# Kernel optimization log

Measured on AMD Instinct MI355X. Metric: run time of the kernel, lower is better.

The kernel has to match this reference:

```python
import jax, jax.numpy as jnp
import numpy as np
import math

N = 20000          # real nodes (batch_size)
D = 256            # hidden_dim
H = 4              # num_heads
L = 3              # num_layers
E = 320000         # local edges
EXP_DEG = 4        # expander_degree
LN_EPS = 1e-5


def setup_inputs() -> dict:
    key = jax.random.key(0)
    ks = jax.random.split(key, 8)
    x = jax.random.normal(ks[0], (N, D), jnp.float32)
    rng = np.random.default_rng(0)
    edge_index = jnp.asarray(rng.integers(0, N, size=(2, E)), dtype=jnp.int32)
    # Expander: EXP_DEG//2 random permutations on N+1 nodes (incl. virtual node),
    # each contributing edges in both directions -> degree-EXP_DEG regular graph.
    n = N + 1
    perms = [rng.permutation(n) for _ in range(EXP_DEG // 2)]
    src = np.concatenate([np.arange(n) for _ in perms] + perms)
    dst = np.concatenate(perms + [np.arange(n) for _ in perms])
    exp_edge_index = jnp.asarray(np.stack([src, dst]), dtype=jnp.int32)
    s_in = 1.0 / math.sqrt(D)
    s_ffn = 1.0 / math.sqrt(4 * D)
    def w(k, shape, s):
        return jax.random.normal(k, shape, jnp.float32) * s
    params = {
        'Wqkv_loc': w(ks[1], (L, D, 3 * D), s_in), 'bqkv_loc': jnp.zeros((L, 3 * D), jnp.float32),
        'Wo_loc':   w(ks[2], (L, D, D), s_in),     'bo_loc':   jnp.zeros((L, D), jnp.float32),
        'Wqkv_exp': w(ks[3], (L, D, 3 * D), s_in), 'bqkv_exp': jnp.zeros((L, 3 * D), jnp.float32),
        'Wo_exp':   w(ks[4], (L, D, D), s_in),     'bo_exp':   jnp.zeros((L, D), jnp.float32),
        'ln_g': jnp.ones((L, D), jnp.float32),     'ln_b': jnp.zeros((L, D), jnp.float32),
        'W1': w(ks[5], (L, D, 4 * D), s_in),       'b1': jnp.zeros((L, 4 * D), jnp.float32),
        'W2': w(ks[6], (L, 4 * D, D), s_ffn),      'b2': jnp.zeros((L, D), jnp.float32),
    }
    return {'x': x, 'edge_index': edge_index, 'exp_edge_index': exp_edge_index, **params}


def _attention(h, src, dst, Wqkv, bqkv, Wo, bo):
    # Sparse multi-head attention over (src -> dst) edges with segment softmax per dst.
    n, d = h.shape
    dh = d // H
    qkv = (h @ Wqkv + bqkv).reshape(n, 3, H, dh)
    q, k, v = qkv[:, 0], qkv[:, 1], qkv[:, 2]            # [n, H, dh]
    score = (q[dst] * k[src]).sum(-1) / jnp.sqrt(jnp.float32(dh))  # [e, H]
    m = jax.ops.segment_max(score, dst, num_segments=n)  # [n, H]
    ex = jnp.exp(score - m[dst])
    denom = jax.ops.segment_sum(ex, dst, num_segments=n)
    alpha = ex / (denom[dst] + 1e-16)
    out = jax.ops.segment_sum(alpha[:, :, None] * v[src], dst, num_segments=n)  # [n, H, dh]
    return out.reshape(n, d) @ Wo + bo


def _layer_norm(x, g, b):
    mu = x.mean(-1, keepdims=True)
    var = ((x - mu) ** 2).mean(-1, keepdims=True)
    return (x - mu) * jax.lax.rsqrt(var + LN_EPS) * g + b


def reference(x, edge_index, exp_edge_index, Wqkv_loc, bqkv_loc, Wo_loc, bo_loc,
              Wqkv_exp, bqkv_exp, Wo_exp, bo_exp, ln_g, ln_b, W1, b1, W2, b2):
    n0 = x.shape[0]
    # VirtualNode transform: append one zero-feature node connected to/from all nodes.
    h = jnp.concatenate([x, jnp.zeros((1, x.shape[1]), x.dtype)], axis=0)
    ar = jnp.arange(n0, dtype=edge_index.dtype)
    vn = jnp.full((n0,), n0, dtype=edge_index.dtype)
    src = jnp.concatenate([edge_index[0], ar, vn])
    dst = jnp.concatenate([edge_index[1], vn, ar])
    esrc, edst = exp_edge_index[0], exp_edge_index[1]
    for l in range(L):  # fixed small number of structurally distinct layers
        res = h
        loc = _attention(h, src, dst, Wqkv_loc[l], bqkv_loc[l], Wo_loc[l], bo_loc[l])
        exp = _attention(h, esrc, edst, Wqkv_exp[l], bqkv_exp[l], Wo_exp[l], bo_exp[l])
        h = _layer_norm(res + loc + exp, ln_g[l], ln_b[l])
        h = h + (jax.nn.gelu(h @ W1[l] + b1[l], approximate=False) @ W2[l] + b2[l])
    return h[:n0]
```

## Files before the change

### kernel.cpp

```cpp
#include <hip/hip_runtime.h>
#include <stdint.h>

#define NREAL   20000
#define NNODES  20001
#define VN      20000
#define E_EDGES 320000
#define NEXP    80004
#define MPAD    20096
#define NVNW    320

typedef unsigned short u16;
typedef unsigned int   u32;
typedef __bf16 bf16x8 __attribute__((ext_vector_type(8)));
typedef float  f32x4  __attribute__((ext_vector_type(4)));
typedef u16    u16x8  __attribute__((ext_vector_type(8)));

__device__ __host__ __forceinline__ size_t fmoff(int row, int col, int LD) {
    return (size_t)(row >> 4) * ((size_t)LD * 16) + (size_t)((col >> 3) * 128)
         + (size_t)((row & 15) * 8) + (size_t)(col & 7);
}

__device__ __forceinline__ int qkv_perm(int n) {
    if (n < 256) return n;
    int u = n - 256;
    int part = u >> 8;
    int cl = u & 255;
    return 256 + (cl >> 2) * 8 + part * 4 + (cl & 3);
}

__device__ __forceinline__ float bf2f(u16 v) {
    union { u32 u; float f; } x; x.u = ((u32)v) << 16; return x.f;
}
__device__ __forceinline__ u16 f2bf(float f) {
    union { float f; u32 u; } x; x.f = f;
    u32 r = (x.u + 0x7fffu + ((x.u >> 16) & 1u)) >> 16;
    return (u16)r;
}
__device__ __forceinline__ float4 cvt4(ushort4 u) {
    return make_float4(bf2f(u.x), bf2f(u.y), bf2f(u.z), bf2f(u.w));
}
__device__ __forceinline__ float4 ld4bf(const u16* p) { return cvt4(*(const ushort4*)p); }
__device__ __forceinline__ float4 cvtk8(u16x8 r) {
    return make_float4(bf2f(r[0]), bf2f(r[1]), bf2f(r[2]), bf2f(r[3]));
}
__device__ __forceinline__ float4 cvtv8(u16x8 r) {
    return make_float4(bf2f(r[4]), bf2f(r[5]), bf2f(r[6]), bf2f(r[7]));
}


__global__ void hinit_kernel(const float* __restrict__ x, float* __restrict__ h,
                             u16* __restrict__ hb) {
    int idx = blockIdx.x * 256 + threadIdx.x;
    if (idx >= NNODES * 64) return;
    int row = idx >> 6, c0 = (idx & 63) * 4;
    float4 v = make_float4(0.f, 0.f, 0.f, 0.f);
    if (row < NREAL) v = *(const float4*)(x + (size_t)row * 256 + c0);
    *(float4*)(h + (size_t)row * 256 + c0) = v;
    ushort4 o;
    o.x = f2bf(v.x); o.y = f2bf(v.y); o.z = f2bf(v.z); o.w = f2bf(v.w);
    *(ushort4*)(hb + fmoff(row, c0, 256)) = o;
}

__global__ void init_kernel(int* cnt, int* fill, int* ecnt,
                            const float* __restrict__ bl, const float* __restrict__ be,
                            float* __restrict__ bcat,
                            const float* __restrict__ bol, const float* __restrict__ boe,
                            float* __restrict__ bsum) {
    int i = blockIdx.x * 256 + threadIdx.x;
    if (i < NREAL) { cnt[i] = 0; fill[i] = 0; }
    if (i < NNODES) ecnt[i] = 0;
    if (i < 3 * 1536) {
        int l = i / 1536, c = i - l * 1536;
        float v = (c < 768) ? bl[l * 768 + c] : be[l * 768 + c - 768];
        int cc = (c >= 768) ? c - 768 : c;
        int d = qkv_perm(cc) + ((c >= 768) ? 768 : 0);
        bcat[l * 1536 + d] = v;
    }
    if (i < 3 * 256) bsum[i] = bol[i] + boe[i];
}

__global__ void csr_count_kernel(const int* __restrict__ ei, int* __restrict__ cnt) {
    int e = blockIdx.x * 256 + threadIdx.x;
    if (e < E_EDGES) atomicAdd(&cnt[ei[E_EDGES + e]], 1);
}

__global__ void csr_scan_kernel(const int* __restrict__ cnt, int* __restrict__ indptr) {
    __shared__ int ssum[256];
    int t = threadIdx.x;
    int c0 = t * 79;
    int s = 0;
    for (int j = 0; j < 79; j++) {
        int i = c0 + j;
        if (i < NREAL) s += cnt[i];
    }
    ssum[t] = s;
    __syncthreads();
    for (int d2 = 1; d2 < 256; d2 <<= 1) {
        int v = (t >= d2) ? ssum[t - d2] : 0;
        __syncthreads();
        ssum[t] += v;
        __syncthreads();
    }
    int run = (t == 0) ? 0 : ssum[t - 1];
    for (int j = 0; j < 79; j++) {
        int i = c0 + j;
        if (i < NREAL) { indptr[i] = run; run += cnt[i]; }
    }
    if (t == 255) indptr[NREAL] = run;
}

__global__ void csr_scatter_kernel(const int* __restrict__ ei, const int* __restrict__ indptr,
                                   int* __restrict__ fill, int* __restrict__ srcs) {
    int e = blockIdx.x * 256 + threadIdx.x;
    if (e < E_EDGES) {
        int d = ei[E_EDGES + e];
        int pos = indptr[d] + atomicAdd(&fill[d], 1);
        srcs[pos] = ei[e];
    }
}

__global__ void exp_scatter_kernel(const int* __restrict__ eei, int* __restrict__ ecnt,
                                   int* __restrict__ esrcs) {
    int e = blockIdx.x * 256 + threadIdx.x;
    if (e < NEXP) {
        int d = eei[NEXP + e];
        int pos = atomicAdd(&ecnt[d], 1);
        esrcs[d * 4 + pos] = eei[e];
    }
}

__global__ void wconv_all_kernel(const float* __restrict__ WqkvL, const float* __restrict__ WqkvE,
                                 const float* __restrict__ WoL, const float* __restrict__ WoE,
                                 const float* __restrict__ W1, const float* __restrict__ W2,
                                 u16* __restrict__ out) {
    int i = blockIdx.x * 256 + threadIdx.x;
    if (i >= 3 * 1048576) return;
    int l = i / 1048576, r = i - l * 1048576;
    if (r >= 393216 && r < 524288) {
        int r2 = r - 393216;
        int k = r2 >> 8, n = r2 & 255;
        float v = (k < 256) ? WoL[(size_t)l * 65536 + k * 256 + n]
                            : WoE[(size_t)l * 65536 + (k - 256) * 256 + n];
        out[(size_t)l * 1048576 + 393216 + fmoff(n, k, 512)] = f2bf(v);
        return;
    }
    const float* src; int K, N; int base;
    if (r < 196608)      { src = WqkvL; K = 256;  N = 768;  base = 0; }
    else if (r < 393216) { src = WqkvE; K = 256;  N = 768;  base = 196608; }
    else if (r < 786432) { src = W1;    K = 256;  N = 1024; base = 524288; }
    else                 { src = W2;    K = 1024; N = 256;  base = 786432; }
    int r2 = r - base;
    int k = r2 / N, n = r2 - k * N;
    int d = (r < 393216) ? qkv_perm(n) : n;
    out[(size_t)l * 1048576 + base + fmoff(d, k, K)] = f2bf(src[(size_t)l * K * N + r2]);
}

template <int EPI>
__global__ __launch_bounds__(256) void gemm_bn(
    const u16* __restrict__ A, const u16* __restrict__ Bt, const float* __restrict__ bias,
    u16* Cb, u16* Q0, u16* KV0, u16* Q1, u16* KV1, int M, int Nout, int nbn) {
    __shared__ u16 lB[128 * 256];
    const int lin = blockIdx.x;
    const int xcd = lin & 7, rest = lin >> 3;
    const int nt = rest % nbn, mc = xcd + 8 * (rest / nbn);
    const int tn = nt * 128;
    const int tid = threadIdx.x;
    const int w = tid >> 6, lane = tid & 63;
    const int lm = lane & 15, q = lane >> 4;

    {
        const u16* bsrc = Bt + (size_t)(tn >> 4) * 4096;
#pragma unroll
        for (int r = 0; r < 16; r++) {
            int o = (r * 256 + tid) * 8;
            *(bf16x8*)&lB[o] = *(const bf16x8*)&bsrc[o];
        }
    }
    __syncthreads();

    f32x4 acc[2][8];
#pragma unroll
    for (int a = 0; a < 2; a++)
#pragma unroll
        for (int b = 0; b < 8; b++) acc[a][b] = (f32x4)0.0f;

    const int lbo = q * 128 + lm * 8;
    const int maxp = MPAD / 16 - 1;

    bf16x8 aS[3][2], bS[2][8];
#pragma unroll
    for (int s = 0; s < 2; s++) {
        int p0 = (mc * 4) * 8 + w * 2;
#pragma unroll
        for (int f = 0; f < 2; f++) {
            int p = p0 + f; if (p > maxp) p = maxp;
            aS[s][f] = *(const bf16x8*)(A + (size_t)p * 4096 + s * 512 + lbo);
        }
#pragma unroll
        for (int n = 0; n < 8; n++)
            bS[s][n] = *(const bf16x8*)&lB[n * 4096 + s * 512 + lbo];
    }

#pragma unroll
    for (int t = 0; t < 32; t++) {
        const int mt = t >> 3, kk = t & 7;
        if (t + 2 < 32) {
            const int t2 = t + 2, mt2 = t2 >> 3, kk2 = t2 & 7;
            int p0 = (mc * 4 + mt2) * 8 + w * 2;
#pragma unroll
            for (int f = 0; f < 2; f++) {
                int p = p0 + f; if (p > maxp) p = maxp;
                aS[t2 % 3][f] = *(const bf16x8*)(A + (size_t)p * 4096 + kk2 * 512 + lbo);
            }
        }
        if (t >= 1 && t + 1 < 32) {
            const int kk1 = (t + 1) & 7;
#pragma unroll
            for (int n = 0; n < 8; n++)
                bS[(t + 1) & 1][n] = *(const bf16x8*)&lB[n * 4096 + kk1 * 512 + lbo];
        }
#pragma unroll
        for (int mi = 0; mi < 2; mi++)
#pragma unroll
            for (int ni = 0; ni < 8; ni++)
                acc[mi][ni] = __builtin_amdgcn_mfma_f32_16x16x32_bf16(
                    bS[t & 1][ni], aS[t % 3][mi], acc[mi][ni], 0, 0, 0);

        if (kk == 7) {
            const int tmg = (mc * 4 + mt) * 128;
#pragma unroll
            for (int mi = 0; mi < 2; mi++) {
                int grow = tmg + w * 32 + mi * 16 + lm;
                if (grow < M) {
#pragma unroll
                    for (int ni = 0; ni < 8; ni++) {
                        int gcol = tn + ni * 16 + q * 4;
                        float4 b4 = *(const float4*)(bias + gcol);
                        float v0 = acc[mi][ni][0] + b4.x;
                        float v1 = acc[mi][ni][1] + b4.y;
                        float v2 = acc[mi][ni][2] + b4.z;
                        float v3 = acc[mi][ni][3] + b4.w;
                        ushort4 o;
                        o.x = f2bf(v0); o.y = f2bf(v1); o.z = f2bf(v2); o.w = f2bf(v3);
                        u16* dst;
                        if (gcol < 256)       dst = Q0  + (size_t)grow * 256 + gcol;
                        else if (gcol < 768)  dst = KV0 + (size_t)grow * 512 + (gcol - 256);
                        else if (gcol < 1024) dst = Q1  + (size_t)grow * 256 + (gcol - 768);
                        else                  dst = KV1 + (size_t)grow * 512 + (gcol - 1024);
                        *(ushort4*)dst = o;
                    }
                }
#pragma unroll
                for (int ni = 0; ni < 8; ni++) acc[mi][ni] = (f32x4)0.0f;
            }
        }
    }
}

__global__ __launch_bounds__(256) void ffn1_rw(
    const u16* __restrict__ A, const u16* __restrict__ Bt, const float* __restrict__ bias,
    u16* __restrict__ Cb, int M) {
    const int lin = blockIdx.x;
    const int mt = lin >> 2, ns = lin & 3;
    const int tm = mt * 64;
    if (tm >= M) return;
    const int tid = threadIdx.x;
    const int w = tid >> 6, lane = tid & 63;
    const int lm = lane & 15, q = lane >> 4;

    f32x4 acc[4][4];
#pragma unroll
    for (int a = 0; a < 4; a++)
#pragma unroll
        for (int b = 0; b < 4; b++) acc[a][b] = (f32x4)0.0f;

    const u16* apf[4];
    const u16* bpf[4];
#pragma unroll
    for (int mi = 0; mi < 4; mi++)
        apf[mi] = A + (size_t)(tm / 16 + mi) * 4096 + q * 128 + lm * 8;
#pragma unroll
    for (int ni = 0; ni < 4; ni++)
        bpf[ni] = Bt + (size_t)(ns * 16 + w * 4 + ni) * 4096 + q * 128 + lm * 8;

    bf16x8 sA[3][4], sB[3][4];
#pragma unroll
    for (int s = 0; s < 2; s++) {
#pragma unroll
        for (int mi = 0; mi < 4; mi++) sA[s][mi] = *(const bf16x8*)(apf[mi] + s * 512);
#pragma unroll
        for (int ni = 0; ni < 4; ni++) sB[s][ni] = *(const bf16x8*)(bpf[ni] + s * 512);
    }
#pragma unroll
    for (int i = 0; i < 8; i++) {
        const int cu = i % 3, pf = (i + 2) % 3;
        if (i + 2 < 8) {
#pragma unroll
            for (int mi = 0; mi < 4; mi++) sA[pf][mi] = *(const bf16x8*)(apf[mi] + (i + 2) * 512);
#pragma unroll
            for (int ni = 0; ni < 4; ni++) sB[pf][ni] = *(const bf16x8*)(bpf[ni] + (i + 2) * 512);
        }
#pragma unroll
        for (int mi = 0; mi < 4; mi++)
#pragma unroll
            for (int ni = 0; ni < 4; ni++)
                acc[mi][ni] = __builtin_amdgcn_mfma_f32_16x16x32_bf16(
                    sB[cu][ni], sA[cu][mi], acc[mi][ni], 0, 0, 0);
    }

    float4 b4[4];
#pragma unroll
    for (int ni = 0; ni < 4; ni++)
        b4[ni] = *(const float4*)(bias + ns * 256 + w * 64 + ni * 16 + q * 4);

#pragma unroll
    for (int mi = 0; mi < 4; mi++) {
        int grow = tm + mi * 16 + lm;
        if (grow >= M) continue;
#pragma unroll
        for (int ni = 0; ni < 4; ni++) {
            int gcol = ns * 256 + w * 64 + ni * 16 + q * 4;
            float v0 = acc[mi][ni][0] + b4[ni].x;
            float v1 = acc[mi][ni][1] + b4[ni].y;
            float v2 = acc[mi][ni][2] + b4[ni].z;
            float v3 = acc[mi][ni][3] + b4[ni].w;
            float g0, g1, g2, g3;
            {
                float u = 0.7978845608f * (v0 + 0.044715f * v0 * v0 * v0);
                g0 = 0.5f * v0 * (2.0f - 2.0f / (__expf(2.0f * u) + 1.0f));
            }
            {
                float u = 0.7978845608f * (v1 + 0.044715f * v1 * v1 * v1);
                g1 = 0.5f * v1 * (2.0f - 2.0f / (__expf(2.0f * u) + 1.0f));
            }
            {
                float u = 0.7978845608f * (v2 + 0.044715f * v2 * v2 * v2);
                g2 = 0.5f * v2 * (2.0f - 2.0f / (__expf(2.0f * u) + 1.0f));
            }
            {
                float u = 0.7978845608f * (v3 + 0.044715f * v3 * v3 * v3);
                g3 = 0.5f * v3 * (2.0f - 2.0f / (__expf(2.0f * u) + 1.0f));
            }
            ushort4 o;
            o.x = f2bf(g0); o.y = f2bf(g1); o.z = f2bf(g2); o.w = f2bf(g3);
            *(ushort4*)(Cb + fmoff(grow, gcol, 1024)) = o;
        }
    }
}

template <int EPI, int K, int MT>
__global__ __launch_bounds__(256) void gemm_fm(
    const u16* __restrict__ A, const u16* __restrict__ Bt, const float* __restrict__ bias,
    u16* Cb, float* Cf, const float* resid, int M, int Nout, int nby) {
    constexpr int MFR = MT / 32;
    constexpr int NK = K / 32;
    const int lin = blockIdx.x;
    const int xcd = lin & 7, sub = lin >> 3;
    const int mtile = xcd + 8 * (sub / nby);
    const int ntile = sub - (sub / nby) * nby;
    const int tm = mtile * MT, tn = ntile * 128;
    if (tm >= M) return;

    const int tid = threadIdx.x;
    const int w = tid >> 6, lane = tid & 63;
    const int lm = lane & 15, q = lane >> 4;
    const int mo = (w >> 1) * (MT / 2), no = (w & 1) * 64;

    f32x4 acc[MFR][4];
#pragma unroll
    for (int a = 0; a < MFR; a++)
#pragma unroll
        for (int b = 0; b < 4; b++) acc[a][b] = (f32x4)0.0f;

    const u16* apf[MFR];
    const u16* bpf[4];
#pragma unroll
    for (int t = 0; t < MFR; t++) {
        int p = (tm + mo) / 16 + t;
        apf[t] = A + (size_t)p * (16 * K) + q * 128 + lm * 8;
    }
#pragma unroll
    for (int n = 0; n < 4; n++) {
        int c = (tn + no) / 16 + n;
        bpf[n] = Bt + (size_t)c * (16 * K) + q * 128 + lm * 8;
    }

    bf16x8 sA[3][MFR], sB[3][4];
#pragma unroll
    for (int s = 0; s < 2 && s < NK; s++) {
#pragma unroll
        for (int t = 0; t < MFR; t++) sA[s][t] = *(const bf16x8*)(apf[t] + s * 512);
#pragma unroll
        for (int n = 0; n < 4; n++) sB[s][n] = *(const bf16x8*)(bpf[n] + s * 512);
    }
#pragma unroll
    for (int i = 0; i < NK; i++) {
        const int cu = i % 3, pf = (i + 2) % 3;
        if (i + 2 < NK) {
#pragma unroll
            for (int t = 0; t < MFR; t++) sA[pf][t] = *(const bf16x8*)(apf[t] + (i + 2) * 512);
#pragma unroll
            for (int n = 0; n < 4; n++) sB[pf][n] = *(const bf16x8*)(bpf[n] + (i + 2) * 512);
        }
#pragma unroll
        for (int mi = 0; mi < MFR; mi++)
#pragma unroll
            for (int ni = 0; ni < 4; ni++)
                acc[mi][ni] = __builtin_amdgcn_mfma_f32_16x16x32_bf16(
                    sB[cu][ni], sA[cu][mi], acc[mi][ni], 0, 0, 0);
    }

    float4 b4[4];
#pragma unroll
    for (int ni = 0; ni < 4; ni++)
        b4[ni] = *(const float4*)(bias + tn + no + ni * 16 + q * 4);

#pragma unroll
    for (int mi = 0; mi < MFR; mi++) {
        int grow = tm + mo + mi * 16 + lm;
        if constexpr (EPI == 4) { if (grow >= NREAL) continue; }
        else                    { if (grow >= M) continue; }
#pragma unroll
        for (int ni = 0; ni < 4; ni++) {
            int gcol = tn + no + ni * 16 + q * 4;
            float v0 = acc[mi][ni][0] + b4[ni].x;
            float v1 = acc[mi][ni][1] + b4[ni].y;
            float v2 = acc[mi][ni][2] + b4[ni].z;
            float v3 = acc[mi][ni][3] + b4[ni].w;
            size_t idx = (size_t)grow * Nout + gcol;
            if constexpr (EPI == 1) {
                *(float4*)(Cf + idx) = make_float4(v0, v1, v2, v3);
            } else if constexpr (EPI == 3) {
                float4 rv = *(const float4*)(resid + idx);
                float o0 = rv.x + v0, o1 = rv.y + v1, o2 = rv.z + v2, o3 = rv.w + v3;
                *(float4*)(Cf + idx) = make_float4(o0, o1, o2, o3);
                ushort4 o;
                o.x = f2bf(o0); o.y = f2bf(o1); o.z = f2bf(o2); o.w = f2bf(o3);
                *(ushort4*)(Cb + fmoff(grow, gcol, Nout)) = o;
            } else {
                float4 rv = *(const float4*)(resid + idx);
                *(float4*)(Cf + idx) = make_float4(rv.x + v0, rv.y + v1, rv.z + v2, rv.w + v3);
            }
        }
    }
}

__global__ void vn_merge_kernel(const float* __restrict__ part, u16* __restrict__ acat) {
    __shared__ float sm[4][64][6];
    int w = threadIdx.x >> 6, lane = threadIdx.x & 63;
    int h = lane >> 4;
    int off = (h << 6) + (lane & 15) * 4;
    float M = -1e30f, L = 0.0f;
    float ax = 0, ay = 0, az = 0, aw = 0;
    for (int p = w * 80; p < w * 80 + 80; p++) {
        const float* pp = part + (size_t)p * 264;
        float pm = pp[h], pl = pp[4 + h];
        float4 nm = *(const float4*)(pp + 8 + off);
        float Mn = fmaxf(M, pm);
        float s0 = __expf(M - Mn);
        float s1 = __expf(pm - Mn);
        ax = ax * s0 + nm.x * s1;
        ay = ay * s0 + nm.y * s1;
        az = az * s0 + nm.z * s1;
        aw = aw * s0 + nm.w * s1;
        L = L * s0 + pl * s1;
        M = Mn;
    }
    sm[w][lane][0] = M; sm[w][lane][1] = L;
    sm[w][lane][2] = ax; sm[w][lane][3] = ay;
    sm[w][lane][4] = az; sm[w][lane][5] = aw;
    __syncthreads();
    if (w == 0) {
        float M2 = -1e30f, L2 = 0.0f;
        float bx = 0, by = 0, bz = 0, bw = 0;
#pragma unroll
        for (int p = 0; p < 4; p++) {
            float pm = sm[p][lane][0], pl = sm[p][lane][1];
            float Mn = fmaxf(M2, pm);
            float s0 = __expf(M2 - Mn);
            float s1 = __expf(pm - Mn);
            bx = bx * s0 + sm[p][lane][2] * s1;
            by = by * s0 + sm[p][lane][3] * s1;
            bz = bz * s0 + sm[p][lane][4] * s1;
            bw = bw * s0 + sm[p][lane][5] * s1;
            L2 = L2 * s0 + pl * s1;
            M2 = Mn;
        }
        float inv = 1.0f / (L2 + 1e-16f);
        ushort4 o;
        o.x = f2bf(bx * inv); o.y = f2bf(by * inv);
        o.z = f2bf(bz * inv); o.w = f2bf(bw * inv);
        *(ushort4*)(acat + fmoff(VN, off, 512)) = o;
    }
}

__global__ void attn_fused_kernel(const u16* __restrict__ qb_loc, const u16* __restrict__ kv_loc,
                                  const u16* __restrict__ qb_exp, const u16* __restrict__ kv_exp,
                                  const int* __restrict__ indptr, const int* __restrict__ srcs,
                                  const int* __restrict__ esrcs,
                                  u16* __restrict__ acat, float* __restrict__ part) {
    int gw0 = (int)((blockIdx.x * (size_t)blockDim.x + threadIdx.x) >> 6);
    int gw = __builtin_amdgcn_readfirstlane(gw0);
    int lane = threadIdx.x & 63;
    int h = lane >> 4;
    int off = (h << 6) + (lane & 15) * 4;
    int coff = (off >> 2) * 8;

    if (gw < NVNW) {
        int wv = gw;
        float4 qv = ld4bf(qb_loc + (size_t)VN * 256 + off);
        float m = -1e30f, l = 0.0f;
        float ax = 0, ay = 0, az = 0, aw = 0;
        for (int i = wv; i < NREAL; i += NVNW) {
            u16x8 r = *(const u16x8*)(kv_loc + (size_t)i * 512 + coff);
            float4 k4 = cvtk8(r);
            float4 v4 = cvtv8(r);
            float s = qv.x * k4.x + qv.y * k4.y + qv.z * k4.z + qv.w * k4.w;
            s += __shfl_xor(s, 1); s += __shfl_xor(s, 2);
            s += __shfl_xor(s, 4); s += __shfl_xor(s, 8);
            float sc = s * 0.125f;
            float mn = fmaxf(m, sc);
            float fold = __expf(m - mn);
            float ee = __expf(sc - mn);
            ax = ax * fold + v4.x * ee;
            ay = ay * fold + v4.y * ee;
            az = az * fold + v4.z * ee;
            aw = aw * fold + v4.w * ee;
            l = l * fold + ee;
            m = mn;
        }
        float* pp = part + (size_t)wv * 264;
        if ((lane & 15) == 0) { pp[h] = m; pp[4 + h] = l; }
        *(float4*)(pp + 8 + off) = make_float4(ax, ay, az, aw);
        return;
    }
    gw -= NVNW;

    const u16 *qb, *kv;
    const int* sl;
    int node, beg, deg, tot, cbase;
    if (gw < NREAL) {
        node = gw; qb = qb_loc; kv = kv_loc; sl = srcs; cbase = 0;
        beg = indptr[node]; deg = indptr[node + 1] - beg; tot = deg + 1;
    } else if (gw < NREAL + NNODES) {
        node = gw - NREAL;
        qb = qb_exp; kv = kv_exp; sl = esrcs; cbase = 256;
        beg = node * 4; deg = 4; tot = 4;
    } else {
        return;
    }

    float4 qv = ld4bf(qb + (size_t)node * 256 + off);
    float m = -1e30f, l = 0.0f;
    float ax = 0, ay = 0, az = 0, aw = 0;

    if (tot <= 4) {
        u16x8 raw[4];
#pragma unroll
        for (int j = 0; j < 4; j++) {
            int s = (j < deg) ? sl[beg + j] : VN;
            raw[j] = *(const u16x8*)(kv + (size_t)s * 512 + coff);
        }
        float sc[4];
#pragma unroll
        for (int j = 0; j < 4; j++) {
            float4 k4 = cvtk8(raw[j]);
            float p = qv.x * k4.x + qv.y * k4.y + qv.z * k4.z + qv.w * k4.w;
            p += __shfl_xor(p, 1); p += __shfl_xor(p, 2);
            p += __shfl_xor(p, 4); p += __shfl_xor(p, 8);
            sc[j] = (j < tot) ? p * 0.125f : -1e30f;
        }
        float mn = fmaxf(fmaxf(sc[0], sc[1]), fmaxf(sc[2], sc[3]));
#pragma unroll
        for (int j = 0; j < 4; j++) {
            float ee = __expf(sc[j] - mn);
            float4 v4 = cvtv8(raw[j]);
            ax += v4.x * ee; ay += v4.y * ee; az += v4.z * ee; aw += v4.w * ee;
            l += ee;
        }
        m = mn;
    } else {
        const int nch = (tot + 7) >> 3;
        u16x8 rA[8], rB[8];
#pragma unroll
        for (int j = 0; j < 8; j++) {
            int s = (j < deg) ? sl[beg + j] : VN;
            rA[j] = *(const u16x8*)(kv + (size_t)s * 512 + coff);
        }
        for (int c = 0; c < nch; c++) {
            if (c + 1 < nch) {
                const int e0n = (c + 1) * 8;
#pragma unroll
                for (int j = 0; j < 8; j++) {
                    int e = e0n + j;
                    int s = (e < deg) ? sl[beg + e] : VN;
                    rB[j] = *(const u16x8*)(kv + (size_t)s * 512 + coff);
                }
            }
            const int e0 = c * 8;
            float sc[8];
#pragma unroll
            for (int j = 0; j < 8; j++) {
                float4 k4 = cvtk8(rA[j]);
                float p = qv.x * k4.x + qv.y * k4.y + qv.z * k4.z + qv.w * k4.w;
                p += __shfl_xor(p, 1); p += __shfl_xor(p, 2);
                p += __shfl_xor(p, 4); p += __shfl_xor(p, 8);
                sc[j] = (e0 + j < tot) ? p * 0.125f : -1e30f;
            }
            float cmax = fmaxf(fmaxf(fmaxf(sc[0], sc[1]), fmaxf(sc[2], sc[3])),
                               fmaxf(fmaxf(sc[4], sc[5]), fmaxf(sc[6], sc[7])));
            float mn = fmaxf(m, cmax);
            float fold = __expf(m - mn);
            ax *= fold; ay *= fold; az *= fold; aw *= fold; l *= fold;
#pragma unroll
            for (int j = 0; j < 8; j++) {
                float ee = __expf(sc[j] - mn);
                float4 v4 = cvtv8(rA[j]);
                ax += v4.x * ee; ay += v4.y * ee; az += v4.z * ee; aw += v4.w * ee;
                l += ee;
            }
            m = mn;
#pragma unroll
            for (int j = 0; j < 8; j++) rA[j] = rB[j];
        }
    }
    float inv = 1.0f / (l + 1e-16f);
    ushort4 o;
    o.x = f2bf(ax * inv); o.y = f2bf(ay * inv);
    o.z = f2bf(az * inv); o.w = f2bf(aw * inv);
    *(ushort4*)(acat + fmoff(node, cbase + off, 512)) = o;
}

__global__ void ln_kernel(const float* hin, const float* __restrict__ asum,
                          const float* __restrict__ g, const float* __restrict__ b,
                          float* hout, u16* __restrict__ hb) {
    int row = blockIdx.x * 4 + (threadIdx.x >> 6);
    if (row >= NNODES) return;
    int lane = threadIdx.x & 63;
    size_t base = (size_t)row * 256 + lane * 4;
    float4 xv = *(const float4*)(hin + base);
    float4 av = *(const float4*)(asum + base);
    xv.x += av.x; xv.y += av.y; xv.z += av.z; xv.w += av.w;
    float s = xv.x + xv.y + xv.z + xv.w;
#pragma unroll
    for (int o = 1; o < 64; o <<= 1) s += __shfl_xor(s, o);
    float mu = s * (1.0f / 256.0f);
    float dx = xv.x - mu, dy = xv.y - mu, dz = xv.z - mu, dw = xv.w - mu;
    float ss = dx * dx + dy * dy + dz * dz + dw * dw;
#pragma unroll
    for (int o = 1; o < 64; o <<= 1) ss += __shfl_xor(ss, o);
    float var = ss * (1.0f / 256.0f);
    float inv = 1.0f / sqrtf(var + 1e-5f);
    float4 gv = *(const float4*)(g + lane * 4);
    float4 bv = *(const float4*)(b + lane * 4);
    float4 y;
    y.x = dx * inv * gv.x + bv.x;
    y.y = dy * inv * gv.y + bv.y;
    y.z = dz * inv * gv.z + bv.z;
    y.w = dw * inv * gv.w + bv.w;
    *(float4*)(hout + base) = y;
    ushort4 o4;
    o4.x = f2bf(y.x); o4.y = f2bf(y.y); o4.z = f2bf(y.z); o4.w = f2bf(y.w);
    *(ushort4*)(hb + fmoff(row, lane * 4, 256)) = o4;
}


extern "C" void kernel_launch(void* const* d_in, const int* in_sizes, int n_in,
                              void* d_out, int out_size, void* d_ws, size_t ws_size,
                              hipStream_t stream) {
    (void)in_sizes; (void)n_in; (void)out_size;
    const float* x        = (const float*)d_in[0];
    const int*   ei       = (const int*)d_in[1];
    const int*   eei      = (const int*)d_in[2];
    const float* Wqkv_loc = (const float*)d_in[3];
    const float* bqkv_loc = (const float*)d_in[4];
    const float* Wo_loc   = (const float*)d_in[5];
    const float* bo_loc   = (const float*)d_in[6];
    const float* Wqkv_exp = (const float*)d_in[7];
    const float* bqkv_exp = (const float*)d_in[8];
    const float* Wo_exp   = (const float*)d_in[9];
    const float* bo_exp   = (const float*)d_in[10];
    const float* ln_g     = (const float*)d_in[11];
    const float* ln_b     = (const float*)d_in[12];
    const float* W1       = (const float*)d_in[13];
    const float* b1       = (const float*)d_in[14];
    const float* W2       = (const float*)d_in[15];
    const float* b2       = (const float*)d_in[16];

    char* wsp = (char*)d_ws;
    size_t off = 0;
    auto carve = [&](size_t bytes) -> void* {
        void* p = wsp + off;
        off += (bytes + 255) & ~(size_t)255;
        return p;
    };
    float* h_f    = (float*)carve((size_t)NNODES * 256 * 4);
    u16*   h_b    = (u16*)carve((size_t)MPAD * 256 * 2);
    u16*   qb_loc = (u16*)carve((size_t)NNODES * 256 * 2);
    u16*   kv_loc = (u16*)carve((size_t)NNODES * 512 * 2);
    u16*   qb_exp = (u16*)carve((size_t)NNODES * 256 * 2);
    u16*   kv_exp = (u16*)carve((size_t)NNODES * 512 * 2);
    u16*   acat   = (u16*)carve((size_t)MPAD * 512 * 2);
    float* asum   = (float*)carve((size_t)NNODES * 256 * 4);
    u16*   wbf    = (u16*)carve((size_t)3 * 1048576 * 2);
    float* bcat   = (float*)carve((size_t)3 * 1536 * 4);
    float* bsum   = (float*)carve((size_t)3 * 256 * 4);
    int*   cnt    = (int*)carve((size_t)NREAL * 4);
    int*   indptr = (int*)carve((size_t)(NREAL + 1) * 4);
    int*   fill   = (int*)carve((size_t)NREAL * 4);
    int*   srcs   = (int*)carve((size_t)E_EDGES * 4);
    int*   ecnt   = (int*)carve((size_t)NNODES * 4);
    int*   esrcs  = (int*)carve((size_t)NNODES * 4 * 4);
    float* part   = (float*)carve((size_t)NVNW * 264 * 4);
    u16*   mid_d  = (u16*)carve((size_t)MPAD * 1024 * 2);
    u16*   mid    = (ws_size >= off) ? mid_d : qb_loc;

    hinit_kernel<<<(NNODES * 64 + 255) / 256, 256, 0, stream>>>(x, h_f, h_b);
    init_kernel<<<(NNODES + 255) / 256, 256, 0, stream>>>(
        cnt, fill, ecnt, bqkv_loc, bqkv_exp, bcat, bo_loc, bo_exp, bsum);
    csr_count_kernel<<<(E_EDGES + 255) / 256, 256, 0, stream>>>(ei, cnt);
    csr_scan_kernel<<<1, 256, 0, stream>>>(cnt, indptr);
    csr_scatter_kernel<<<(E_EDGES + 255) / 256, 256, 0, stream>>>(ei, indptr, fill, srcs);
    exp_scatter_kernel<<<(NEXP + 255) / 256, 256, 0, stream>>>(eei, ecnt, esrcs);
    wconv_all_kernel<<<(3 * 1048576 + 255) / 256, 256, 0, stream>>>(
        Wqkv_loc, Wqkv_exp, Wo_loc, Wo_exp, W1, W2, wbf);

    const int NBM64 = 320;
    const int ATTN_BLOCKS = (NVNW + NREAL + NNODES + 3) / 4;

    for (int l = 0; l < 3; l++) {
        const u16* wqkvC = wbf + (size_t)l * 1048576 + 0;
        const u16* wocat = wbf + (size_t)l * 1048576 + 393216;
        const u16* w1T   = wbf + (size_t)l * 1048576 + 524288;
        const u16* w2T   = wbf + (size_t)l * 1048576 + 786432;

        gemm_bn<6><<<480, 256, 0, stream>>>(
            h_b, wqkvC, bcat + l * 1536, nullptr,
            qb_loc, kv_loc, qb_exp, kv_exp, NNODES, 1536, 12);

        attn_fused_kernel<<<ATTN_BLOCKS, 256, 0, stream>>>(
            qb_loc, kv_loc, qb_exp, kv_exp, indptr, srcs, esrcs, acat, part);
        vn_merge_kernel<<<1, 256, 0, stream>>>(part, acat);

        gemm_fm<1, 512, 64><<<NBM64 * 2, 256, 0, stream>>>(
            acat, wocat, bsum + l * 256, nullptr, asum, nullptr, NNODES, 256, 2);

        ln_kernel<<<(NNODES + 3) / 4, 256, 0, stream>>>(
            h_f, asum, ln_g + l * 256, ln_b + l * 256, h_f, h_b);

        ffn1_rw<<<320 * 4, 256, 0, stream>>>(
            h_b, w1T, b1 + l * 1024, mid, NNODES);

        if (l < 2) {
            gemm_fm<3, 1024, 64><<<NBM64 * 2, 256, 0, stream>>>(
                mid, w2T, b2 + l * 256, h_b, h_f, h_f, NNODES, 256, 2);
        } else {
            gemm_fm<4, 1024, 64><<<NBM64 * 2, 256, 0, stream>>>(
                mid, w2T, b2 + l * 256, nullptr, (float*)d_out, h_f, NNODES, 256, 2);
        }
    }
}
```

Before: 798.2 us.

## Replace LDS-staged QKV GEMM with register-direct 64x256 tile kernel

The QKV projection GEMM no longer stages a 128-column weight slab in shared memory for a persistent block that loops over several M tiles. It becomes a kernel with many small blocks, each computing a 64-row by 256-column tile and loading both A and B fragments straight from global memory into registers with a three-stage prefetch. This removes the LDS staging and barrier and raises the block count for better occupancy. In exchange, weights are re-read from global memory or cache by every block.

```diff
diff --git a/kernel.cpp b/kernel.cpp
--- a/kernel.cpp
+++ b/kernel.cpp
@@ -155,104 +155,82 @@
     out[(size_t)l * 1048576 + base + fmoff(d, k, K)] = f2bf(src[(size_t)l * K * N + r2]);
 }
 
-template <int EPI>
-__global__ __launch_bounds__(256) void gemm_bn(
+__global__ __launch_bounds__(256) void qkv_rw(
     const u16* __restrict__ A, const u16* __restrict__ Bt, const float* __restrict__ bias,
-    u16* Cb, u16* Q0, u16* KV0, u16* Q1, u16* KV1, int M, int Nout, int nbn) {
-    __shared__ u16 lB[128 * 256];
+    u16* __restrict__ Q0, u16* __restrict__ KV0,
+    u16* __restrict__ Q1, u16* __restrict__ KV1, int M) {
     const int lin = blockIdx.x;
-    const int xcd = lin & 7, rest = lin >> 3;
-    const int nt = rest % nbn, mc = xcd + 8 * (rest / nbn);
-    const int tn = nt * 128;
+    const int mt = lin / 6, ns = lin - mt * 6;
+    const int tm = mt * 64;
+    if (tm >= M) return;
     const int tid = threadIdx.x;
     const int w = tid >> 6, lane = tid & 63;
     const int lm = lane & 15, q = lane >> 4;
 
-    {
-        const u16* bsrc = Bt + (size_t)(tn >> 4) * 4096;
-#pragma unroll
-        for (int r = 0; r < 16; r++) {
-            int o = (r * 256 + tid) * 8;
-            *(bf16x8*)&lB[o] = *(const bf16x8*)&bsrc[o];
-        }
-    }
-    __syncthreads();
-
-    f32x4 acc[2][8];
-#pragma unroll
-    for (int a = 0; a < 2; a++)
-#pragma unroll
-        for (int b = 0; b < 8; b++) acc[a][b] = (f32x4)0.0f;
-
-    const int lbo = q * 128 + lm * 8;
-    const int maxp = MPAD / 16 - 1;
-
-    bf16x8 aS[3][2], bS[2][8];
+    f32x4 acc[4][4];
+#pragma unroll
+    for (int a = 0; a < 4; a++)
+#pragma unroll
+        for (int b = 0; b < 4; b++) acc[a][b] = (f32x4)0.0f;
+
+    const u16* apf[4];
+    const u16* bpf[4];
+#pragma unroll
+    for (int mi = 0; mi < 4; mi++)
+        apf[mi] = A + (size_t)(tm / 16 + mi) * 4096 + q * 128 + lm * 8;
+#pragma unroll
+    for (int ni = 0; ni < 4; ni++)
+        bpf[ni] = Bt + (size_t)(ns * 16 + w * 4 + ni) * 4096 + q * 128 + lm * 8;
+
+    bf16x8 sA[3][4], sB[3][4];
 #pragma unroll
     for (int s = 0; s < 2; s++) {
-        int p0 = (mc * 4) * 8 + w * 2;
-#pragma unroll
-        for (int f = 0; f < 2; f++) {
-            int p = p0 + f; if (p > maxp) p = maxp;
-            aS[s][f] = *(const bf16x8*)(A + (size_t)p * 4096 + s * 512 + lbo);
-        }
-#pragma unroll
-        for (int n = 0; n < 8; n++)
-            bS[s][n] = *(const bf16x8*)&lB[n * 4096 + s * 512 + lbo];
-    }
-
-#pragma unroll
-    for (int t = 0; t < 32; t++) {
-        const int mt = t >> 3, kk = t & 7;
-        if (t + 2 < 32) {
-            const int t2 = t + 2, mt2 = t2 >> 3, kk2 = t2 & 7;
-            int p0 = (mc * 4 + mt2) * 8 + w * 2;
-#pragma unroll
-            for (int f = 0; f < 2; f++) {
-                int p = p0 + f; if (p > maxp) p = maxp;
-                aS[t2 % 3][f] = *(const bf16x8*)(A + (size_t)p * 4096 + kk2 * 512 + lbo);
-            }
-        }
-        if (t >= 1 && t + 1 < 32) {
-            const int kk1 = (t + 1) & 7;
-#pragma unroll
-            for (int n = 0; n < 8; n++)
-                bS[(t + 1) & 1][n] = *(const bf16x8*)&lB[n * 4096 + kk1 * 512 + lbo];
-        }
-#pragma unroll
-        for (int mi = 0; mi < 2; mi++)
-#pragma unroll
-            for (int ni = 0; ni < 8; ni++)
+#pragma unroll
+        for (int mi = 0; mi < 4; mi++) sA[s][mi] = *(const bf16x8*)(apf[mi] + s * 512);
+#pragma unroll
+        for (int ni = 0; ni < 4; ni++) sB[s][ni] = *(const bf16x8*)(bpf[ni] + s * 512);
+    }
+#pragma unroll
+    for (int i = 0; i < 8; i++) {
+        const int cu = i % 3, pf = (i + 2) % 3;
+        if (i + 2 < 8) {
+#pragma unroll
+            for (int mi = 0; mi < 4; mi++) sA[pf][mi] = *(const bf16x8*)(apf[mi] + (i + 2) * 512);
+#pragma unroll
+            for (int ni = 0; ni < 4; ni++) sB[pf][ni] = *(const bf16x8*)(bpf[ni] + (i + 2) * 512);
+        }
+#pragma unroll
+        for (int mi = 0; mi < 4; mi++)
+#pragma unroll
+            for (int ni = 0; ni < 4; ni++)
                 acc[mi][ni] = __builtin_amdgcn_mfma_f32_16x16x32_bf16(
-                    bS[t & 1][ni], aS[t % 3][mi], acc[mi][ni], 0, 0, 0);
-
-        if (kk == 7) {
-            const int tmg = (mc * 4 + mt) * 128;
-#pragma unroll
-            for (int mi = 0; mi < 2; mi++) {
-                int grow = tmg + w * 32 + mi * 16 + lm;
-                if (grow < M) {
-#pragma unroll
-                    for (int ni = 0; ni < 8; ni++) {
-                        int gcol = tn + ni * 16 + q * 4;
-                        float4 b4 = *(const float4*)(bias + gcol);
-                        float v0 = acc[mi][ni][0] + b4.x;
-                        float v1 = acc[mi][ni][1] + b4.y;
-                        float v2 = acc[mi][ni][2] + b4.z;
-                        float v3 = acc[mi][ni][3] + b4.w;
-                        ushort4 o;
-                        o.x = f2bf(v0); o.y = f2bf(v1); o.z = f2bf(v2); o.w = f2bf(v3);
-                        u16* dst;
-                        if (gcol < 256)       dst = Q0  + (size_t)grow * 256 + gcol;
-                        else if (gcol < 768)  dst = KV0 + (size_t)grow * 512 + (gcol - 256);
-                        else if (gcol < 1024) dst = Q1  + (size_t)grow * 256 + (gcol - 768);
-                        else                  dst = KV1 + (size_t)grow * 512 + (gcol - 1024);
-                        *(ushort4*)dst = o;
-                    }
-                }
-#pragma unroll
-                for (int ni = 0; ni < 8; ni++) acc[mi][ni] = (f32x4)0.0f;
-            }
+                    sB[cu][ni], sA[cu][mi], acc[mi][ni], 0, 0, 0);
+    }
+
+    float4 b4[4];
+#pragma unroll
+    for (int ni = 0; ni < 4; ni++)
+        b4[ni] = *(const float4*)(bias + ns * 256 + w * 64 + ni * 16 + q * 4);
+
+#pragma unroll
+    for (int mi = 0; mi < 4; mi++) {
+        int grow = tm + mi * 16 + lm;
+        if (grow >= M) continue;
+#pragma unroll
+        for (int ni = 0; ni < 4; ni++) {
+            int gcol = ns * 256 + w * 64 + ni * 16 + q * 4;
+            float v0 = acc[mi][ni][0] + b4[ni].x;
+            float v1 = acc[mi][ni][1] + b4[ni].y;
+            float v2 = acc[mi][ni][2] + b4[ni].z;
+            float v3 = acc[mi][ni][3] + b4[ni].w;
+            ushort4 o;
+            o.x = f2bf(v0); o.y = f2bf(v1); o.z = f2bf(v2); o.w = f2bf(v3);
+            u16* dst;
+            if (gcol < 256)       dst = Q0  + (size_t)grow * 256 + gcol;
+            else if (gcol < 768)  dst = KV0 + (size_t)grow * 512 + (gcol - 256);
+            else if (gcol < 1024) dst = Q1  + (size_t)grow * 256 + (gcol - 768);
+            else                  dst = KV1 + (size_t)grow * 512 + (gcol - 1024);
+            *(ushort4*)dst = o;
         }
     }
 }
@@ -727,6 +705,7 @@
 
     const int NBM64 = 320;
     const int ATTN_BLOCKS = (NVNW + NREAL + NNODES + 3) / 4;
+    const int QKV_BLOCKS = (MPAD / 64) * 6;
 
     for (int l = 0; l < 3; l++) {
         const u16* wqkvC = wbf + (size_t)l * 1048576 + 0;
@@ -734,9 +713,9 @@
         const u16* w1T   = wbf + (size_t)l * 1048576 + 524288;
         const u16* w2T   = wbf + (size_t)l * 1048576 + 786432;
 
-        gemm_bn<6><<<480, 256, 0, stream>>>(
-            h_b, wqkvC, bcat + l * 1536, nullptr,
-            qb_loc, kv_loc, qb_exp, kv_exp, NNODES, 1536, 12);
+        qkv_rw<<<QKV_BLOCKS, 256, 0, stream>>>(
+            h_b, wqkvC, bcat + l * 1536,
+            qb_loc, kv_loc, qb_exp, kv_exp, NNODES);
 
         attn_fused_kernel<<<ATTN_BLOCKS, 256, 0, stream>>>(
             qb_loc, kv_loc, qb_exp, kv_exp, indptr, srcs, esrcs, acat, part);
```

New measurement: 822.8 us. 1.03x slower.
